# Kernel optimization log

Measured on AMD Instinct MI355X. Metric: run time of the kernel, lower is better.

Reference implementation:

```python
import jax
import jax.numpy as jnp
from jax import lax
import numpy as np

# module hyperparameters (match init_kwargs)
IN_C, OUT_C = 32, 64
K, STRIDE, PAD, DIL = 3, 1, 1, 1
GRID_SIZE, ORDER = 5, 3
GRID_LO, GRID_HI = -1.0, 1.0
SCALE_SPLINE = 1.0
EPS = 1e-8


def _knot_grid():
    # grid = arange(-order, grid_size+order+1) * h + lo ; length = grid_size + 2*order + 1 = 12
    h = (GRID_HI - GRID_LO) / GRID_SIZE
    return jnp.arange(-ORDER, GRID_SIZE + ORDER + 1, dtype=jnp.float32) * h + GRID_LO


def _bspline_bases(x):
    """Cox-de Boor recursion. x: (N, P) -> bases: (N, P, GRID_SIZE+ORDER)."""
    grid = _knot_grid()
    xe = x[..., None]  # (N, P, 1)
    bases = ((xe >= grid[:-1]) & (xe < grid[1:])).astype(x.dtype)  # (N, P, 11)
    for k in range(1, ORDER + 1):
        left_den = jnp.maximum(grid[k:-1] - grid[:-(k + 1)], EPS)
        right_den = jnp.maximum(grid[k + 1:] - grid[1:-k], EPS)
        bases = ((xe - grid[:-(k + 1)]) / left_den * bases[..., :-1]
                 + (grid[k + 1:] - xe) / right_den * bases[..., 1:])
    return bases  # (N, P, 8)


def setup_inputs() -> dict:
    key = jax.random.key(0)
    k1, k2, k3 = jax.random.split(key, 3)
    x = jax.random.normal(k1, (4, IN_C, 56, 56), dtype=jnp.float32)
    base_weight = jax.random.normal(k2, (OUT_C, IN_C, K, K), dtype=jnp.float32) * 0.05
    spline_weight = jax.random.normal(k3, (OUT_C, IN_C * K * K, GRID_SIZE + ORDER), dtype=jnp.float32) * 0.05
    spline_scaler = jnp.ones((OUT_C,), dtype=jnp.float32)
    return {"x": x, "base_weight": base_weight,
            "spline_weight": spline_weight, "spline_scaler": spline_scaler}


def reference(x, base_weight, spline_weight, spline_scaler):
    B, C, H, W = x.shape
    pad = [(PAD, PAD), (PAD, PAD)]
    # base path: conv2d -> SiLU
    base_conv = lax.conv_general_dilated(
        x, base_weight, window_strides=(STRIDE, STRIDE), padding=pad,
        rhs_dilation=(DIL, DIL), dimension_numbers=("NCHW", "OIHW", "NCHW"))
    base_out = jax.nn.silu(base_conv)

    # unfold: (B, C*K*K, oh, ow) with torch Unfold channel ordering (c, kh, kw)
    patches = lax.conv_general_dilated_patches(
        x, filter_shape=(K, K), window_strides=(STRIDE, STRIDE), padding=pad,
        rhs_dilation=(DIL, DIL))
    oh, ow = patches.shape[2], patches.shape[3]
    num_patches = oh * ow
    # (B*num_patches, C*K*K)
    pf = patches.reshape(B, C * K * K, num_patches).transpose(0, 2, 1).reshape(-1, C * K * K)

    bases = _bspline_bases(pf)  # (N, P, F)
    # contract patch-dim and basis-dim against spline weights
    spl = jnp.einsum("npf,opf->no", bases, spline_weight) * spline_scaler  # (N, O)
    spl = spl.reshape(B, num_patches, OUT_C).transpose(0, 2, 1).reshape(B, OUT_C, oh, ow)
    return base_out + SCALE_SPLINE * spl
```

## Files before the change

### kernel.cpp

```cpp
#include <hip/hip_runtime.h>
#include <math.h>


typedef __attribute__((ext_vector_type(8))) short bf16x8;
typedef __attribute__((ext_vector_type(4))) float f32x4;

#define MFMA16(a, b, c) __builtin_amdgcn_mfma_f32_16x16x32_bf16((a), (b), (c), 0, 0, 0)

__device__ __forceinline__ unsigned short f2bf(float f) {
    unsigned u = __builtin_bit_cast(unsigned, f);
    u = (u + 0x7fffu + ((u >> 16) & 1u)) >> 16;
    return (unsigned short)u;
}

__device__ __forceinline__ void eval_bases(float v, float bs[8]) {
    #pragma unroll
    for (int i = 0; i < 8; ++i) bs[i] = 0.0f;
    float t = (v + 2.2f) * 2.5f;
    if (t >= 0.0f && t < 11.0f) {
        int j = (int)t;
        if (j > 10) j = 10;
        float knot = (float)(j - 3) * 0.4f - 1.0f;
        float u  = (v - knot) * 2.5f;
        float um = 1.0f - u;
        float u2 = u * u, u3 = u2 * u;
        const float s6 = 1.0f / 6.0f;
        float w0 = um * um * um * s6;
        float w1 = (3.0f * u3 - 6.0f * u2 + 4.0f) * s6;
        float w2 = (-3.0f * u3 + 3.0f * u2 + 3.0f * u + 1.0f) * s6;
        float w3 = u3 * s6;
        int i0 = j - 3;
        if (i0 >= 0)               bs[i0]     = w0;
        if (i0 + 1 >= 0 && i0 < 7) bs[i0 + 1] = w1;
        if (i0 + 2 >= 0 && i0 < 6) bs[i0 + 2] = w2;
        if (i0 + 3 <= 7)           bs[i0 + 3] = w3;
    }
}

__global__ __launch_bounds__(256)
void cvt_swz_kernel(const float* __restrict__ ws, const float* __restrict__ wb,
                    unsigned short* __restrict__ wst, unsigned short* __restrict__ wbt) {
    int i = blockIdx.x * 256 + threadIdx.x;
    if (i < 147456) {
        int j = i & 7, l = (i >> 3) & 63, t = i >> 9;
        int S = t % 72, nq = t / 72;
        int oc = nq * 16 + (l & 15);
        int k  = S * 32 + (l >> 4) * 8 + j;
        wst[i] = f2bf(ws[oc * 2304 + k]);
    } else {
        int i2 = i - 147456;
        if (i2 < 18432) {
            int j = i2 & 7, l = (i2 >> 3) & 63, t = i2 >> 9;
            int s = t % 9, nq = t / 9;
            int oc = nq * 16 + (l & 15);
            int k  = s * 32 + (l >> 4) * 8 + j;
            wbt[i2] = f2bf(wb[oc * 288 + k]);
        }
    }
}

__global__ __launch_bounds__(512)
void kan_mfma_kernel(const float* __restrict__ x,
                     const float* __restrict__ sc,
                     const unsigned short* __restrict__ wst,
                     const unsigned short* __restrict__ wbt,
                     float* __restrict__ out) {
    __shared__ unsigned short smem[24832];
    unsigned short* sb    = smem;
    unsigned short* patch = smem + 15360;

    const int tid = threadIdx.x;
    const int bx  = blockIdx.x;
    const int b   = bx / 98;
    const int r   = bx - b * 98;
    const int ty  = r / 7;
    const int tx  = r - ty * 7;
    const int h0  = ty * 4, w0 = tx * 8;

    const int lane = tid & 63;
    const int wv   = tid >> 6;
    const int nq   = wv & 3;
    const int mh   = wv >> 2;
    const int ml   = lane & 15;
    const int kg   = lane >> 4;
    const int m    = mh * 16 + ml;
    const int py0  = m >> 3, px0 = m & 7;

    float vv[4];
    #pragma unroll
    for (int j = 0; j < 4; ++j) {
        int i = tid + j * 512;
        float val = 0.0f;
        if (i < 1920) {
            int c  = i / 60;
            int hp = i - c * 60;
            int hy = hp / 10;
            int hx = hp - hy * 10;
            int hh = h0 + hy - 1, ww = w0 + hx - 1;
            if ((unsigned)hh < 56u && (unsigned)ww < 56u)
                val = x[((b * 32 + c) * 56 + hh) * 56 + ww];
        }
        vv[j] = val;
    }
    #pragma unroll
    for (int j = 0; j < 4; ++j) {
        int i = tid + j * 512;
        if (i < 1920) {
            int c  = i / 60;
            int hp = i - c * 60;
            int hy = hp / 10;
            int hx = hp - hy * 10;
            float bs[8];
            eval_bases(vv[j], bs);
            bf16x8 pk;
            #pragma unroll
            for (int j2 = 0; j2 < 8; ++j2) pk[j2] = (short)f2bf(bs[j2]);
            *reinterpret_cast<bf16x8*>(&sb[i * 8]) = pk;
            unsigned short xb = f2bf(vv[j]);
            #pragma unroll
            for (int kh = 0; kh < 3; ++kh) {
                int py = hy - kh;
                if ((unsigned)py < 4u) {
                    #pragma unroll
                    for (int kw = 0; kw < 3; ++kw) {
                        int px = hx - kw;
                        if ((unsigned)px < 8u)
                            patch[(py * 8 + px) * 296 + c * 9 + kh * 3 + kw] = xb;
                    }
                }
            }
        }
    }
    __syncthreads();

    int aoff[9];
    #pragma unroll
    for (int u = 0; u < 9; ++u) {
        int tt  = 4 * u + kg;
        int dc  = tt / 9;
        int tap = tt - dc * 9;
        int kh  = tap / 3;
        int kw  = tap - kh * 3;
        aoff[u] = (dc * 60 + (py0 + kh) * 10 + (px0 + kw)) * 8;
    }

    f32x4 accS = {0.f, 0.f, 0.f, 0.f};
    f32x4 accB = {0.f, 0.f, 0.f, 0.f};

    const unsigned short* bp = wst + (nq * 72 * 64 + lane) * 8;
    int cbase = 0;
    for (int g = 0; g < 8; ++g) {
        #pragma unroll
        for (int u = 0; u < 9; ++u) {
            bf16x8 a  = *reinterpret_cast<const bf16x8*>(&sb[cbase + aoff[u]]);
            bf16x8 bw = *reinterpret_cast<const bf16x8*>(bp + (g * 9 + u) * 512);
            accS = MFMA16(a, bw, accS);
        }
        cbase += 1920;
    }

    {
        const unsigned short* ap  = patch + m * 296 + kg * 8;
        const unsigned short* bbp = wbt + (nq * 9 * 64 + lane) * 8;
        #pragma unroll
        for (int s = 0; s < 9; ++s) {
            bf16x8 a  = *reinterpret_cast<const bf16x8*>(ap + s * 32);
            bf16x8 bw = *reinterpret_cast<const bf16x8*>(bbp + s * 512);
            accB = MFMA16(a, bw, accB);
        }
    }

    const int oc  = nq * 16 + ml;
    const float scv = sc[oc];
    const int rowb = mh * 16 + kg * 4;
    const int py   = rowb >> 3;
    const int pxb  = rowb & 7;
    float* ob = out + ((b * 64 + oc) * 56 + h0 + py) * 56 + w0 + pxb;
    f32x4 res;
    #pragma unroll
    for (int reg = 0; reg < 4; ++reg) {
        float bv = accB[reg];
        float si = bv / (1.0f + __expf(-bv));
        res[reg] = si + scv * accS[reg];
    }
    *reinterpret_cast<f32x4*>(ob) = res;
}

extern "C" void kernel_launch(void* const* d_in, const int* in_sizes, int n_in,
                              void* d_out, int out_size, void* d_ws, size_t ws_size,
                              hipStream_t stream) {
    const float* x  = (const float*)d_in[0];
    const float* wb = (const float*)d_in[1];
    const float* ws = (const float*)d_in[2];
    const float* sc = (const float*)d_in[3];
    float* out = (float*)d_out;

    unsigned short* wst = (unsigned short*)d_ws;
    unsigned short* wbt = wst + 147456;

    cvt_swz_kernel<<<648, 256, 0, stream>>>(ws, wb, wst, wbt);
    kan_mfma_kernel<<<392, 512, 0, stream>>>(x, sc, wst, wbt, out);
}
```

Measured before the change: 78.91 us.

## Split K across wave halves and reuse B fragments for two M tiles

Each wave now computes both 16-row M tiles, so every loaded weight fragment feeds two MFMAs. The two wave groups instead split the reduction dimension: channel groups for the spline GEMM and tap steps for the base GEMM. Partial sums are combined through shared memory, which needs an extra barrier pair and makes half the waves idle during the epilogue. The aim is to halve global/L2 weight traffic per MFMA, at the cost of extra synchronisation and LDS traffic for the reduction.

```diff
diff --git a/kernel.cpp b/kernel.cpp
--- a/kernel.cpp
+++ b/kernel.cpp
@@ -80,11 +80,10 @@
     const int lane = tid & 63;
     const int wv   = tid >> 6;
     const int nq   = wv & 3;
-    const int mh   = wv >> 2;
+    const int kh   = wv >> 2;
     const int ml   = lane & 15;
     const int kg   = lane >> 4;
-    const int m    = mh * 16 + ml;
-    const int py0  = m >> 3, px0 = m & 7;
+    const int py0  = ml >> 3, px0 = ml & 7;
 
     float vv[4];
     #pragma unroll
@@ -118,14 +117,14 @@
             *reinterpret_cast<bf16x8*>(&sb[i * 8]) = pk;
             unsigned short xb = f2bf(vv[j]);
             #pragma unroll
-            for (int kh = 0; kh < 3; ++kh) {
-                int py = hy - kh;
+            for (int dkh = 0; dkh < 3; ++dkh) {
+                int py = hy - dkh;
                 if ((unsigned)py < 4u) {
                     #pragma unroll
-                    for (int kw = 0; kw < 3; ++kw) {
-                        int px = hx - kw;
+                    for (int dkw = 0; dkw < 3; ++dkw) {
+                        int px = hx - dkw;
                         if ((unsigned)px < 8u)
-                            patch[(py * 8 + px) * 296 + c * 9 + kh * 3 + kw] = xb;
+                            patch[(py * 8 + px) * 296 + c * 9 + dkh * 3 + dkw] = xb;
                     }
                 }
             }
@@ -139,51 +138,89 @@
         int tt  = 4 * u + kg;
         int dc  = tt / 9;
         int tap = tt - dc * 9;
-        int kh  = tap / 3;
-        int kw  = tap - kh * 3;
-        aoff[u] = (dc * 60 + (py0 + kh) * 10 + (px0 + kw)) * 8;
-    }
-
-    f32x4 accS = {0.f, 0.f, 0.f, 0.f};
-    f32x4 accB = {0.f, 0.f, 0.f, 0.f};
-
-    const unsigned short* bp = wst + (nq * 72 * 64 + lane) * 8;
-    int cbase = 0;
-    for (int g = 0; g < 8; ++g) {
+        int th  = tap / 3;
+        int tw  = tap - th * 3;
+        aoff[u] = (dc * 60 + (py0 + th) * 10 + (px0 + tw)) * 8;
+    }
+
+    f32x4 accS0 = {0.f, 0.f, 0.f, 0.f};
+    f32x4 accS1 = {0.f, 0.f, 0.f, 0.f};
+    f32x4 accB0 = {0.f, 0.f, 0.f, 0.f};
+    f32x4 accB1 = {0.f, 0.f, 0.f, 0.f};
+
+    const unsigned short* bp = wst + ((nq * 72 + kh * 36) * 64 + lane) * 8;
+    int cbase = kh * 4 * 1920;
+    for (int g = 0; g < 4; ++g) {
         #pragma unroll
         for (int u = 0; u < 9; ++u) {
-            bf16x8 a  = *reinterpret_cast<const bf16x8*>(&sb[cbase + aoff[u]]);
+            bf16x8 a0 = *reinterpret_cast<const bf16x8*>(&sb[cbase + aoff[u]]);
+            bf16x8 a1 = *reinterpret_cast<const bf16x8*>(&sb[cbase + aoff[u] + 160]);
             bf16x8 bw = *reinterpret_cast<const bf16x8*>(bp + (g * 9 + u) * 512);
-            accS = MFMA16(a, bw, accS);
+            accS0 = MFMA16(a0, bw, accS0);
+            accS1 = MFMA16(a1, bw, accS1);
         }
         cbase += 1920;
     }
 
     {
-        const unsigned short* ap  = patch + m * 296 + kg * 8;
+        const unsigned short* ap0 = patch + ml * 296 + kg * 8;
+        const unsigned short* ap1 = ap0 + 16 * 296;
         const unsigned short* bbp = wbt + (nq * 9 * 64 + lane) * 8;
-        #pragma unroll
-        for (int s = 0; s < 9; ++s) {
-            bf16x8 a  = *reinterpret_cast<const bf16x8*>(ap + s * 32);
+        const int sbeg = kh ? 5 : 0;
+        const int send = kh ? 9 : 5;
+        for (int s = sbeg; s < send; ++s) {
+            bf16x8 a0 = *reinterpret_cast<const bf16x8*>(ap0 + s * 32);
+            bf16x8 a1 = *reinterpret_cast<const bf16x8*>(ap1 + s * 32);
             bf16x8 bw = *reinterpret_cast<const bf16x8*>(bbp + s * 512);
-            accB = MFMA16(a, bw, accB);
-        }
-    }
-
-    const int oc  = nq * 16 + ml;
-    const float scv = sc[oc];
-    const int rowb = mh * 16 + kg * 4;
-    const int py   = rowb >> 3;
-    const int pxb  = rowb & 7;
-    float* ob = out + ((b * 64 + oc) * 56 + h0 + py) * 56 + w0 + pxb;
-    f32x4 res;
-    #pragma unroll
-    for (int reg = 0; reg < 4; ++reg) {
-        float bv = accB[reg];
-        float si = bv / (1.0f + __expf(-bv));
-        res[reg] = si + scv * accS[reg];
-    }
-    *reinterpret_cast<f32x4*>(ob) = res;
+            accB0 = MFMA16(a0, bw, accB0);
+            accB1 = MFMA16(a1, bw, accB1);
+        }
+    }
+
+    __syncthreads();
+    float* red = reinterpret_cast<float*>(smem);
+    const int idx = nq * 64 + lane;
+    if (kh) {
+        #pragma unroll
+        for (int w = 0; w < 4; ++w) red[(0  + w) * 260 + idx] = accS0[w];
+        #pragma unroll
+        for (int w = 0; w < 4; ++w) red[(4  + w) * 260 + idx] = accS1[w];
+        #pragma unroll
+        for (int w = 0; w < 4; ++w) red[(8  + w) * 260 + idx] = accB0[w];
+        #pragma unroll
+        for (int w = 0; w < 4; ++w) red[(12 + w) * 260 + idx] = accB1[w];
+    }
+    __syncthreads();
+    if (!kh) {
+        #pragma unroll
+        for (int w = 0; w < 4; ++w) accS0[w] += red[(0  + w) * 260 + idx];
+        #pragma unroll
+        for (int w = 0; w < 4; ++w) accS1[w] += red[(4  + w) * 260 + idx];
+        #pragma unroll
+        for (int w = 0; w < 4; ++w) accB0[w] += red[(8  + w) * 260 + idx];
+        #pragma unroll
+        for (int w = 0; w < 4; ++w) accB1[w] += red[(12 + w) * 260 + idx];
+
+        const int oc  = nq * 16 + ml;
+        const float scv = sc[oc];
+        #pragma unroll
+        for (int f = 0; f < 2; ++f) {
+            const int rowb = f * 16 + kg * 4;
+            const int py   = rowb >> 3;
+            const int pxb  = rowb & 7;
+            float* ob = out + ((b * 64 + oc) * 56 + h0 + py) * 56 + w0 + pxb;
+            f32x4 aB = f ? accB1 : accB0;
+            f32x4 aS = f ? accS1 : accS0;
+            f32x4 res;
+            #pragma unroll
+            for (int reg = 0; reg < 4; ++reg) {
+                float bv = aB[reg];
+                float si = bv / (1.0f + __expf(-bv));
+                res[reg] = si + scv * aS[reg];
+            }
+            *reinterpret_cast<f32x4*>(ob) = res;
+        }
+    }
 }
 
 extern "C" void kernel_launch(void* const* d_in, const int* in_sizes, int n_in,
```

Result: no change. 77.60 us (-1.7%).
